# Kernel optimization log

Hardware: AMD Instinct MI355X
Metric: run time of the kernel (lower is better)

Reference implementation:

```python
import jax, jax.numpy as jnp
import numpy as np

PENALTY_FACTOR = 2.0
THRESHOLD = 0.01
PHASE_INT_THRESHOLD = 0.01  # hard-coded 0.01 in the original forward


def setup_inputs() -> dict:
    key = jax.random.key(0)
    k1, k2, k3 = jax.random.split(key, 3)
    B, twoN = 1024, 65536
    prediction = jax.random.normal(k1, (B, twoN), dtype=jnp.float32)
    label = jax.random.normal(k2, (B, twoN), dtype=jnp.float32)
    spectrogram = jax.random.normal(k3, (B, 128, 128), dtype=jnp.float32)
    return {"prediction": prediction, "label": label, "spectrogram": spectrogram}


def _significant_bounds(mask, n):
    # mask: [B, N] bool. first/last index where mask is True; (0, n-1) if none.
    idx = jnp.arange(n)
    any_ = jnp.any(mask, axis=1, keepdims=True)
    first = jnp.min(jnp.where(mask, idx, n), axis=1, keepdims=True)
    last = jnp.max(jnp.where(mask, idx, -1), axis=1, keepdims=True)
    first = jnp.where(any_, first, 0)
    last = jnp.where(any_, last, n - 1)
    return first, last  # each [B, 1]


def reference(prediction, label, spectrogram):
    B, two_n = label.shape
    n = two_n // 2
    label_real, label_imag = label[:, :n], label[:, n:]
    pred_real, pred_imag = prediction[:, :n], prediction[:, n:]

    label_phase = jnp.arctan2(label_imag, label_real)
    pred_phase = jnp.arctan2(pred_imag, pred_real)
    label_int = label_real ** 2 + label_imag ** 2
    pred_int = pred_real ** 2 + pred_imag ** 2

    idx = jnp.arange(n)[None, :]  # [1, N]
    fr, lr = _significant_bounds(jnp.abs(label_real) > THRESHOLD, n)
    fi, li = _significant_bounds(jnp.abs(label_imag) > THRESHOLD, n)

    # penalty applied outside the significant region [first, last]
    scale_r = jnp.where((idx < fr) | (idx > lr), PENALTY_FACTOR, 1.0)
    scale_i = jnp.where((idx < fi) | (idx > li), PENALTY_FACTOR, 1.0)

    mse_real = (pred_real - label_real) ** 2 * scale_r
    mse_imag = (pred_imag - label_imag) ** 2 * scale_i
    mse_int = (pred_int - label_int) ** 2
    mse_phase = jnp.where(jnp.abs(label_int) < PHASE_INT_THRESHOLD,
                          0.0, (pred_phase - label_phase) ** 2)

    per_sample = (mse_real.mean(axis=1) + mse_imag.mean(axis=1)
                  + 10.0 * mse_int.mean(axis=1) + 5.0 * mse_phase.mean(axis=1))
    return per_sample.mean()
```

## Files before the change

### kernel.cpp

```cpp
#include <hip/hip_runtime.h>
#include <math.h>

#define SIG_THRESHOLD 0.01f
#define PHASE_INT_THR 0.01f

typedef float f32x2 __attribute__((ext_vector_type(2)));

__device__ __forceinline__ f32x2 phase_term_pair(f32x2 lr, f32x2 li, f32x2 pr, f32x2 pi,
                                                 f32x2 lint) {
    f32x2 cross = pi * lr - pr * li;
    f32x2 dotv  = pr * lr + pi * li;

    f32x2 ax = __builtin_elementwise_abs(dotv);
    f32x2 ay = __builtin_elementwise_abs(cross);
    f32x2 mx = __builtin_elementwise_max(ax, ay);
    f32x2 mn = __builtin_elementwise_min(ax, ay);
    f32x2 rcp;
    rcp.x = __builtin_amdgcn_rcpf(mx.x);
    rcp.y = __builtin_amdgcn_rcpf(mx.y);
    f32x2 t = mn * rcp;
    t.x = (mx.x == 0.0f) ? 0.0f : t.x;
    t.y = (mx.y == 0.0f) ? 0.0f : t.y;

    f32x2 s = t * t;
    f32x2 p = s * (-0.01172120f) + 0.05265332f;
    p = s * p + (-0.11643287f);
    p = s * p + 0.19354346f;
    p = s * p + (-0.33262347f);
    p = s * p + 0.99997726f;
    f32x2 r = p * t;

    f32x2 rq  = 1.57079632679f - r;
    r.x = (ay.x > ax.x) ? rq.x : r.x;
    r.y = (ay.y > ax.y) ? rq.y : r.y;
    f32x2 rpi = 3.14159265359f - r;
    r.x = (dotv.x < 0.0f) ? rpi.x : r.x;
    r.y = (dotv.y < 0.0f) ? rpi.y : r.y;
    r.x = copysignf(r.x, cross.x);
    r.y = copysignf(r.y, cross.y);

    float sg0, sg1;
    {
        bool php = pi.x > 0.0f, phl = li.x > 0.0f;
        sg0 = (php && !phl && r.x < 0.0f) ? 1.0f
            : ((!php && phl && r.x > 0.0f) ? -1.0f : 0.0f);
        php = pi.y > 0.0f; phl = li.y > 0.0f;
        sg1 = (php && !phl && r.y < 0.0f) ? 1.0f
            : ((!php && phl && r.y > 0.0f) ? -1.0f : 0.0f);
    }
    f32x2 sg; sg.x = sg0; sg.y = sg1;
    f32x2 dph2 = sg * (12.566370614f * r + 39.4784176044f * sg) + r * r;

    dph2.x = (lint.x >= PHASE_INT_THR) ? dph2.x : 0.0f;
    dph2.y = (lint.y >= PHASE_INT_THR) ? dph2.y : 0.0f;
    return dph2;
}

__device__ __forceinline__ void process_pair(f32x2 lr, f32x2 li, f32x2 pr, f32x2 pi,
                                             f32x2& sr, f32x2& si, f32x2& sint, f32x2& sph) {
    f32x2 dr = pr - lr;  sr += dr * dr;
    f32x2 di = pi - li;  si += di * di;
    f32x2 lint = lr * lr + li * li;
    f32x2 pint = pr * pr + pi * pi;
    f32x2 dint = pint - lint;  sint += dint * dint;
    sph += phase_term_pair(lr, li, pr, pi, lint);
}


__device__ __forceinline__ float4 waveReduceSum4(float4 v) {
#pragma unroll
    for (int o = 32; o > 0; o >>= 1) {
        v.x += __shfl_down(v.x, o, 64);
        v.y += __shfl_down(v.y, o, 64);
        v.z += __shfl_down(v.z, o, 64);
        v.w += __shfl_down(v.w, o, 64);
    }
    return v;
}

__device__ __forceinline__ int4 waveReduceBounds(int4 v) {
#pragma unroll
    for (int o = 32; o > 0; o >>= 1) {
        v.x = min(v.x, __shfl_down(v.x, o, 64));
        v.y = max(v.y, __shfl_down(v.y, o, 64));
        v.z = min(v.z, __shfl_down(v.z, o, 64));
        v.w = max(v.w, __shfl_down(v.w, o, 64));
    }
    return v;
}

__device__ __forceinline__ float4 blockReduceSum4(float4 v, float4* lds4) {
    __syncthreads();
    v = waveReduceSum4(v);
    int lane = threadIdx.x & 63, wave = threadIdx.x >> 6;
    if (lane == 0) lds4[wave] = v;
    __syncthreads();
    int nw = blockDim.x >> 6;
    float4 r = (threadIdx.x < nw) ? lds4[threadIdx.x] : make_float4(0.f, 0.f, 0.f, 0.f);
    if (threadIdx.x < 64) r = waveReduceSum4(r);
    if (threadIdx.x == 0) lds4[0] = r;
    __syncthreads();
    return lds4[0];
}

#define COARSE_SENT (1 << 29)

__device__ __forceinline__ int4 blockReduceBounds(int4 v, int4* ldsi4) {
    __syncthreads();
    v = waveReduceBounds(v);
    int lane = threadIdx.x & 63, wave = threadIdx.x >> 6;
    if (lane == 0) ldsi4[wave] = v;
    __syncthreads();
    int nw = blockDim.x >> 6;
    int4 r = (threadIdx.x < nw) ? ldsi4[threadIdx.x]
                                : make_int4(COARSE_SENT, -1, COARSE_SENT, -1);
    if (threadIdx.x < 64) r = waveReduceBounds(r);
    if (threadIdx.x == 0) ldsi4[0] = r;
    __syncthreads();
    return ldsi4[0];
}

__global__ void __launch_bounds__(512)
prl_row_kernel(const float* __restrict__ pred, const float* __restrict__ label,
               float* __restrict__ row_out, int n, int two_n) {
    __shared__ float4 s_f4[8];
    __shared__ int4 s_i4[8];
    __shared__ int s_b[4];

    const int row = blockIdx.x;
    const float* __restrict__ P = pred  + (size_t)row * two_n;
    const float* __restrict__ L = label + (size_t)row * two_n;
    const int tid = threadIdx.x;
    const int nt  = blockDim.x;

    const float4* __restrict__ Lr4 = reinterpret_cast<const float4*>(L);
    const float4* __restrict__ Li4 = reinterpret_cast<const float4*>(L + n);
    const float4* __restrict__ Pr4 = reinterpret_cast<const float4*>(P);
    const float4* __restrict__ Pi4 = reinterpret_cast<const float4*>(P + n);

    f32x2 sr = {0.f, 0.f}, si = {0.f, 0.f}, sint = {0.f, 0.f}, sph = {0.f, 0.f};
    int4 bounds = make_int4(COARSE_SENT, -1, COARSE_SENT, -1);

    const int nvec = n / 4;
    for (int v = tid; v < nvec; v += nt) {
        float4 a = Lr4[v], b = Li4[v], c = Pr4[v], d = Pi4[v];

        f32x2 lr0; lr0.x = a.x; lr0.y = a.y;
        f32x2 lr1; lr1.x = a.z; lr1.y = a.w;
        f32x2 li0; li0.x = b.x; li0.y = b.y;
        f32x2 li1; li1.x = b.z; li1.y = b.w;
        f32x2 pr0; pr0.x = c.x; pr0.y = c.y;
        f32x2 pr1; pr1.x = c.z; pr1.y = c.w;
        f32x2 pi0; pi0.x = d.x; pi0.y = d.y;
        f32x2 pi1; pi1.x = d.z; pi1.y = d.w;

        process_pair(lr0, li0, pr0, pi0, sr, si, sint, sph);
        process_pair(lr1, li1, pr1, pi1, sr, si, sint, sph);

        float amr = fmaxf(fmaxf(fmaxf(fabsf(a.x), fabsf(a.y)), fabsf(a.z)), fabsf(a.w));
        float ami = fmaxf(fmaxf(fmaxf(fabsf(b.x), fabsf(b.y)), fabsf(b.z)), fabsf(b.w));
        bool srb = amr > SIG_THRESHOLD;
        bool sib = ami > SIG_THRESHOLD;
        bounds.x = min(bounds.x, srb ? v : COARSE_SENT);
        bounds.y = srb ? v : bounds.y;
        bounds.z = min(bounds.z, sib ? v : COARSE_SENT);
        bounds.w = sib ? v : bounds.w;
    }

    float4 sums = make_float4(sr.x + sr.y, si.x + si.y, sint.x + sint.y, sph.x + sph.y);
    float4 tot = blockReduceSum4(sums, s_f4);
    int4 b4 = blockReduceBounds(bounds, s_i4);

    if (tid < 4) s_b[tid] = (tid & 1) ? -1 : n;
    __syncthreads();
    if (tid < 16) {
        int which = tid >> 2;
        int k = tid & 3;
        const float* base = (which >= 2) ? (L + n) : L;
        int v4 = (which == 0) ? b4.x : (which == 1) ? b4.y : (which == 2) ? b4.z : b4.w;
        bool valid = (which & 1) ? (v4 >= 0) : (v4 < COARSE_SENT);
        if (valid) {
            int idx = v4 * 4 + k;
            if (fabsf(base[idx]) > SIG_THRESHOLD) {
                if (which & 1) atomicMax(&s_b[which], idx);
                else           atomicMin(&s_b[which], idx);
            }
        }
    }
    __syncthreads();
    int fr = s_b[0], lr = s_b[1], fi = s_b[2], li = s_b[3];
    if (fr == n) { fr = 0; lr = n - 1; }
    if (fi == n) { fi = 0; li = n - 1; }

    float4 osum = make_float4(0.f, 0.f, 0.f, 0.f);
    for (int i = tid; i < fr; i += nt)          { float d = P[i] - L[i];         osum.x = fmaf(d, d, osum.x); }
    for (int i = lr + 1 + tid; i < n; i += nt)  { float d = P[i] - L[i];         osum.x = fmaf(d, d, osum.x); }
    for (int i = tid; i < fi; i += nt)          { float d = P[n + i] - L[n + i]; osum.y = fmaf(d, d, osum.y); }
    for (int i = li + 1 + tid; i < n; i += nt)  { float d = P[n + i] - L[n + i]; osum.y = fmaf(d, d, osum.y); }

    float4 otot = blockReduceSum4(osum, s_f4);

    if (tid == 0) {
        float wr = tot.x + otot.x;
        float wi = tot.y + otot.y;
        row_out[row] = (wr + wi + 10.0f * tot.z + 5.0f * tot.w) / (float)n;
    }
}

__global__ void __launch_bounds__(1024)
prl_finalize_kernel(const float* __restrict__ rows, float* __restrict__ out, int B) {
    __shared__ float4 s_f4[16];
    float4 v = make_float4(0.f, 0.f, 0.f, 0.f);
    for (int i = threadIdx.x; i < B; i += blockDim.x) v.x += rows[i];
    __syncthreads();
    v = waveReduceSum4(v);
    int lane = threadIdx.x & 63, wave = threadIdx.x >> 6;
    if (lane == 0) s_f4[wave] = v;
    __syncthreads();
    int nw = blockDim.x >> 6;
    float4 r = (threadIdx.x < nw) ? s_f4[threadIdx.x] : make_float4(0.f, 0.f, 0.f, 0.f);
    if (threadIdx.x < 64) r = waveReduceSum4(r);
    if (threadIdx.x == 0) out[0] = r.x / (float)B;
}

extern "C" void kernel_launch(void* const* d_in, const int* in_sizes, int n_in,
                              void* d_out, int out_size, void* d_ws, size_t ws_size,
                              hipStream_t stream) {
    const float* pred  = (const float*)d_in[0];
    const float* label = (const float*)d_in[1];

    const int B     = in_sizes[2] / (128 * 128);
    const int two_n = in_sizes[0] / B;
    const int n     = two_n / 2;

    float* row_out = (float*)d_ws;
    float* out     = (float*)d_out;

    prl_row_kernel<<<B, 512, 0, stream>>>(pred, label, row_out, n, two_n);
    prl_finalize_kernel<<<1, 1024, 0, stream>>>(row_out, out, B);
}
```

Before: 111.9 us.

## Software-pipeline row loads with inline-asm double-buffered dwordx4 and manual waitcnt

For the default shape (n/4 == 16*blockDim), the streaming loop is fully unrolled into a double-buffered schedule. Raw global_load_dwordx4 asm keeps 16 vector loads in flight, and explicit s_waitcnt vmcnt lets compute on one buffer overlap the loads for the next. The aim is more memory-level parallelism per wave for this bandwidth-bound reduction. It also adds a waves_per_eu hint and keeps a generic fallback loop, at the cost of higher VGPR use and a more fragile, hand-scheduled code path.

```diff
diff --git a/kernel.cpp b/kernel.cpp
--- a/kernel.cpp
+++ b/kernel.cpp
@@ -5,6 +5,16 @@
 #define PHASE_INT_THR 0.01f
 
 typedef float f32x2 __attribute__((ext_vector_type(2)));
+typedef float f32x4 __attribute__((ext_vector_type(4)));
+
+__device__ __forceinline__ void gl4(const f32x4* p, f32x4& d) {
+    asm volatile("global_load_dwordx4 %0, %1, off" : "=v"(d) : "v"(p));
+}
+template<int N>
+__device__ __forceinline__ void wait_vm() {
+    asm volatile("s_waitcnt vmcnt(%0)" :: "i"(N) : "memory");
+    __builtin_amdgcn_sched_barrier(0);
+}
 
 __device__ __forceinline__ f32x2 phase_term_pair(f32x2 lr, f32x2 li, f32x2 pr, f32x2 pi,
                                                  f32x2 lint) {
@@ -66,6 +76,33 @@
     sph += phase_term_pair(lr, li, pr, pi, lint);
 }
 
+#define COARSE_SENT (1 << 29)
+
+__device__ __forceinline__ void process_quad(f32x4 a, f32x4 b, f32x4 c, f32x4 d, int v,
+                                             f32x2& sr, f32x2& si, f32x2& sint, f32x2& sph,
+                                             int4& bounds) {
+    f32x2 lr0; lr0.x = a.x; lr0.y = a.y;
+    f32x2 lr1; lr1.x = a.z; lr1.y = a.w;
+    f32x2 li0; li0.x = b.x; li0.y = b.y;
+    f32x2 li1; li1.x = b.z; li1.y = b.w;
+    f32x2 pr0; pr0.x = c.x; pr0.y = c.y;
+    f32x2 pr1; pr1.x = c.z; pr1.y = c.w;
+    f32x2 pi0; pi0.x = d.x; pi0.y = d.y;
+    f32x2 pi1; pi1.x = d.z; pi1.y = d.w;
+
+    process_pair(lr0, li0, pr0, pi0, sr, si, sint, sph);
+    process_pair(lr1, li1, pr1, pi1, sr, si, sint, sph);
+
+    float amr = fmaxf(fmaxf(fmaxf(fabsf(a.x), fabsf(a.y)), fabsf(a.z)), fabsf(a.w));
+    float ami = fmaxf(fmaxf(fmaxf(fabsf(b.x), fabsf(b.y)), fabsf(b.z)), fabsf(b.w));
+    bool srb = amr > SIG_THRESHOLD;
+    bool sib = ami > SIG_THRESHOLD;
+    bounds.x = min(bounds.x, srb ? v : COARSE_SENT);
+    bounds.y = srb ? v : bounds.y;
+    bounds.z = min(bounds.z, sib ? v : COARSE_SENT);
+    bounds.w = sib ? v : bounds.w;
+}
+
 
 __device__ __forceinline__ float4 waveReduceSum4(float4 v) {
 #pragma unroll
@@ -103,8 +140,6 @@
     return lds4[0];
 }
 
-#define COARSE_SENT (1 << 29)
-
 __device__ __forceinline__ int4 blockReduceBounds(int4 v, int4* ldsi4) {
     __syncthreads();
     v = waveReduceBounds(v);
@@ -120,7 +155,17 @@
     return ldsi4[0];
 }
 
-__global__ void __launch_bounds__(512)
+#define IG(X, vb) \
+    gl4(Lr4v + (vb), X##0); gl4(Li4v + (vb), X##1); \
+    gl4(Pr4v + (vb), X##2); gl4(Pi4v + (vb), X##3); \
+    gl4(Lr4v + (vb) + nt, X##4); gl4(Li4v + (vb) + nt, X##5); \
+    gl4(Pr4v + (vb) + nt, X##6); gl4(Pi4v + (vb) + nt, X##7);
+
+#define CG(X, vb) \
+    process_quad(X##0, X##1, X##2, X##3, (vb), sr, si, sint, sph, bounds); \
+    process_quad(X##4, X##5, X##6, X##7, (vb) + nt, sr, si, sint, sph, bounds);
+
+__global__ void __launch_bounds__(512) __attribute__((amdgpu_waves_per_eu(2, 4)))
 prl_row_kernel(const float* __restrict__ pred, const float* __restrict__ label,
                float* __restrict__ row_out, int n, int two_n) {
     __shared__ float4 s_f4[8];
@@ -133,38 +178,40 @@
     const int tid = threadIdx.x;
     const int nt  = blockDim.x;
 
-    const float4* __restrict__ Lr4 = reinterpret_cast<const float4*>(L);
-    const float4* __restrict__ Li4 = reinterpret_cast<const float4*>(L + n);
-    const float4* __restrict__ Pr4 = reinterpret_cast<const float4*>(P);
-    const float4* __restrict__ Pi4 = reinterpret_cast<const float4*>(P + n);
-
     f32x2 sr = {0.f, 0.f}, si = {0.f, 0.f}, sint = {0.f, 0.f}, sph = {0.f, 0.f};
     int4 bounds = make_int4(COARSE_SENT, -1, COARSE_SENT, -1);
 
     const int nvec = n / 4;
-    for (int v = tid; v < nvec; v += nt) {
-        float4 a = Lr4[v], b = Li4[v], c = Pr4[v], d = Pi4[v];
-
-        f32x2 lr0; lr0.x = a.x; lr0.y = a.y;
-        f32x2 lr1; lr1.x = a.z; lr1.y = a.w;
-        f32x2 li0; li0.x = b.x; li0.y = b.y;
-        f32x2 li1; li1.x = b.z; li1.y = b.w;
-        f32x2 pr0; pr0.x = c.x; pr0.y = c.y;
-        f32x2 pr1; pr1.x = c.z; pr1.y = c.w;
-        f32x2 pi0; pi0.x = d.x; pi0.y = d.y;
-        f32x2 pi1; pi1.x = d.z; pi1.y = d.w;
-
-        process_pair(lr0, li0, pr0, pi0, sr, si, sint, sph);
-        process_pair(lr1, li1, pr1, pi1, sr, si, sint, sph);
-
-        float amr = fmaxf(fmaxf(fmaxf(fabsf(a.x), fabsf(a.y)), fabsf(a.z)), fabsf(a.w));
-        float ami = fmaxf(fmaxf(fmaxf(fabsf(b.x), fabsf(b.y)), fabsf(b.z)), fabsf(b.w));
-        bool srb = amr > SIG_THRESHOLD;
-        bool sib = ami > SIG_THRESHOLD;
-        bounds.x = min(bounds.x, srb ? v : COARSE_SENT);
-        bounds.y = srb ? v : bounds.y;
-        bounds.z = min(bounds.z, sib ? v : COARSE_SENT);
-        bounds.w = sib ? v : bounds.w;
+
+    if (nvec == 16 * nt) {
+        const f32x4* Lr4v = reinterpret_cast<const f32x4*>(L);
+        const f32x4* Li4v = reinterpret_cast<const f32x4*>(L + n);
+        const f32x4* Pr4v = reinterpret_cast<const f32x4*>(P);
+        const f32x4* Pi4v = reinterpret_cast<const f32x4*>(P + n);
+
+        f32x4 A0, A1, A2, A3, A4, A5, A6, A7;
+        f32x4 B0, B1, B2, B3, B4, B5, B6, B7;
+
+        IG(A, tid);
+        IG(B, tid + 2 * nt);
+
+        wait_vm<8>();  CG(A, tid);              IG(A, tid + 4 * nt);
+        wait_vm<8>();  CG(B, tid + 2 * nt);     IG(B, tid + 6 * nt);
+        wait_vm<8>();  CG(A, tid + 4 * nt);     IG(A, tid + 8 * nt);
+        wait_vm<8>();  CG(B, tid + 6 * nt);     IG(B, tid + 10 * nt);
+        wait_vm<8>();  CG(A, tid + 8 * nt);     IG(A, tid + 12 * nt);
+        wait_vm<8>();  CG(B, tid + 10 * nt);    IG(B, tid + 14 * nt);
+        wait_vm<8>();  CG(A, tid + 12 * nt);
+        wait_vm<0>();  CG(B, tid + 14 * nt);
+    } else {
+        const f32x4* Lr4v = reinterpret_cast<const f32x4*>(L);
+        const f32x4* Li4v = reinterpret_cast<const f32x4*>(L + n);
+        const f32x4* Pr4v = reinterpret_cast<const f32x4*>(P);
+        const f32x4* Pi4v = reinterpret_cast<const f32x4*>(P + n);
+        for (int v = tid; v < nvec; v += nt) {
+            f32x4 a = Lr4v[v], b = Li4v[v], c = Pr4v[v], d = Pi4v[v];
+            process_quad(a, b, c, d, v, sr, si, sint, sph, bounds);
+        }
     }
 
     float4 sums = make_float4(sr.x + sr.y, si.x + si.y, sint.x + sint.y, sph.x + sph.y);
```

Result: faster. 109.0 us (-2.5%).
